# Kernel optimization log

Hardware: AMD Instinct MI355X
Metric: run time of the kernel (lower is better)

The kernel has to match this reference:

```python
import jax, jax.numpy as jnp
import numpy as np

N = 100_000      # nodes
E = 1_600_000    # edges (avg degree 16)
F_IN = 128       # num_features
HID = 64         # width
C = 40           # num_classes


def setup_inputs() -> dict:
    key = jax.random.key(0)
    ks = jax.random.split(key, 8)
    x = jax.random.normal(ks[0], (N, F_IN), jnp.float32)
    edge_index = jax.random.randint(ks[1], (2, E), 0, N, dtype=jnp.int32)
    # Xavier-uniform-like scaled weights (matches nn.init.xavier_uniform_ statistics)
    def xavier(k, fan_in, fan_out):
        lim = np.sqrt(6.0 / (fan_in + fan_out)).astype(np.float32)
        return jax.random.uniform(k, (fan_in, fan_out), jnp.float32, -lim, lim)
    return {
        "x": x,
        "edge_index": edge_index,
        "W1": xavier(ks[2], F_IN, HID), "b1": jnp.zeros((HID,), jnp.float32),
        "W2": xavier(ks[3], HID, HID),  "b2": jnp.zeros((HID,), jnp.float32),
        "W3": xavier(ks[4], HID, C),    "b3": jnp.zeros((C,), jnp.float32),
    }


def _gcn_forward(x, edge_index, W1, b1, W2, b2, W3, b3):
    n = x.shape[0]
    loops = jnp.arange(n, dtype=edge_index.dtype)
    src = jnp.concatenate([edge_index[0], loops])  # row (source)
    dst = jnp.concatenate([edge_index[1], loops])  # col (target)
    # symmetric GCN normalization with self-loops (PyG gcn_norm, edge_weight=1)
    deg = jax.ops.segment_sum(jnp.ones_like(dst, x.dtype), dst, num_segments=n)
    dis = jnp.where(deg > 0, jax.lax.rsqrt(jnp.maximum(deg, 1e-12)), 0.0)
    norm = (dis[src] * dis[dst])[:, None]  # [E+N, 1]

    def conv(h, W, b):
        h = h @ W                                                   # [n, out]
        agg = jax.ops.segment_sum(h[src] * norm, dst, num_segments=n)
        return agg + b

    h = conv(x, W1, b1)
    h = h * jax.nn.sigmoid(h)   # swish
    h = conv(h, W2, b2)
    h = h * jax.nn.sigmoid(h)   # swish
    return jax.nn.log_softmax(conv(h, W3, b3), axis=1)


def reference(x, edge_index, W1, b1, W2, b2, W3, b3):
    return _gcn_forward(x, edge_index, W1, b1, W2, b2, W3, b3)
```

## Files before the change

kernel.cpp:

```cpp
#include <hip/hip_runtime.h>
#include <math.h>

#define THREADS 256
#define S1THREADS 512
#define BSHIFT 9
#define BSIZE (1 << BSHIFT)
#define PASS1_CHUNK 2048
#define SRC_BITS 17
#define S2CAP 12288

typedef unsigned int u32;
typedef unsigned short u16;
typedef __attribute__((ext_vector_type(8))) short short8v;
typedef __attribute__((ext_vector_type(4))) float float4v;

__device__ __forceinline__ u16 f2bf(float f) {
    u32 u = __float_as_uint(f);
    u = (u + 0x7fffu + ((u >> 16) & 1u)) >> 16;
    return (u16)u;
}
__device__ __forceinline__ float bf_lo(u32 u) { return __uint_as_float(u << 16); }
__device__ __forceinline__ float bf_hi(u32 u) { return __uint_as_float(u & 0xffff0000u); }


__global__ __launch_bounds__(THREADS) void bzero_kernel(int* __restrict__ bcnt, int nbuck) {
    int i = threadIdx.x;
    if (i < nbuck) bcnt[i] = 0;
}

__global__ __launch_bounds__(THREADS) void bhist_kernel(const int* __restrict__ dst,
                                                        int* __restrict__ bcnt, int e, int nbuck) {
    __shared__ int hist[BSIZE];
    const int tid = threadIdx.x;
    const int c0  = blockIdx.x * PASS1_CHUNK;
    for (int i = tid; i < nbuck; i += THREADS) hist[i] = 0;
    __syncthreads();
    for (int i = tid; i < PASS1_CHUNK; i += THREADS) {
        int idx = c0 + i;
        if (idx < e) atomicAdd(&hist[dst[idx] >> BSHIFT], 1);
    }
    __syncthreads();
    for (int b = tid; b < nbuck; b += THREADS) {
        int h = hist[b];
        if (h) atomicAdd(&bcnt[b], h);
    }
}

__global__ __launch_bounds__(1024) void bscan_kernel(const int* __restrict__ bcnt,
                                                     int* __restrict__ bbase,
                                                     int* __restrict__ pcur,
                                                     int* __restrict__ rowptr,
                                                     int nbuck, int n, int e) {
    __shared__ int s[1024];
    int v = (threadIdx.x < nbuck) ? bcnt[threadIdx.x] : 0;
    s[threadIdx.x] = v;
    __syncthreads();
    for (int off = 1; off < 1024; off <<= 1) {
        int t = (threadIdx.x >= off) ? s[threadIdx.x - off] : 0;
        __syncthreads();
        s[threadIdx.x] += t;
        __syncthreads();
    }
    if (threadIdx.x < nbuck) {
        int ex = s[threadIdx.x] - v;
        bbase[threadIdx.x] = ex;
        pcur[threadIdx.x]  = ex;
    }
    if (threadIdx.x == 0) { bbase[nbuck] = e; rowptr[n] = e; }
}


__global__ __launch_bounds__(S1THREADS) void sort1_kernel(
    const int* __restrict__ src, const int* __restrict__ dst,
    int* __restrict__ pcur, u32* __restrict__ pairs, int e, int nbuck)
{
    __shared__ int hist[BSIZE], hist2[BSIZE], base_s[BSIZE];
    const int tid = threadIdx.x;
    const int c0  = blockIdx.x * PASS1_CHUNK;
    for (int i = tid; i < nbuck; i += S1THREADS) { hist[i] = 0; hist2[i] = 0; }
    __syncthreads();
    for (int i = tid; i < PASS1_CHUNK; i += S1THREADS) {
        int idx = c0 + i;
        if (idx < e) atomicAdd(&hist[dst[idx] >> BSHIFT], 1);
    }
    __syncthreads();
    for (int b = tid; b < nbuck; b += S1THREADS) {
        int h = hist[b];
        base_s[b] = h ? atomicAdd(&pcur[b], h) : 0;
    }
    __syncthreads();
    for (int i = tid; i < PASS1_CHUNK; i += S1THREADS) {
        int idx = c0 + i;
        if (idx < e) {
            int d = dst[idx];
            int b = d >> BSHIFT;
            int off = atomicAdd(&hist2[b], 1);
            pairs[base_s[b] + off] = ((u32)(d & (BSIZE - 1)) << SRC_BITS) | (u32)src[idx];
        }
    }
}


__global__ __launch_bounds__(S1THREADS) void sort2_kernel(
    const int* __restrict__ bbase, const u32* __restrict__ pairs,
    int* __restrict__ rowptr, float* __restrict__ dis,
    int* __restrict__ csr, int n)
{
    __shared__ int cnt[BSIZE];
    __shared__ int cur[BSIZE];
    __shared__ int s2[S1THREADS];
    __shared__ u32 pst[S2CAP];

    const int b  = blockIdx.x;
    const int d0 = b << BSHIFT;
    const int nd = min(BSIZE, n - d0);
    const int p0 = bbase[b], p1 = bbase[b + 1];
    const int sz = p1 - p0;
    const int tid = threadIdx.x;

    for (int i = tid; i < BSIZE; i += S1THREADS) cnt[i] = 0;
    __syncthreads();

    for (int j = tid; j < sz; j += S1THREADS) {
        u32 pr = pairs[p0 + j];
        if (j < S2CAP) pst[j] = pr;
        atomicAdd(&cnt[pr >> SRC_BITS], 1);
    }
    __syncthreads();

    int v = cnt[tid];
    s2[tid] = v;
    __syncthreads();
    for (int off = 1; off < S1THREADS; off <<= 1) {
        int t = (tid >= off) ? s2[tid - off] : 0;
        __syncthreads();
        s2[tid] += t;
        __syncthreads();
    }
    cur[tid] = p0 + s2[tid] - v;
    __syncthreads();

    for (int i = tid; i < nd; i += S1THREADS) {
        rowptr[d0 + i] = cur[i];
        dis[d0 + i] = rsqrtf((float)(cnt[i] + 1));
    }
    __syncthreads();

    for (int j = tid; j < sz; j += S1THREADS) {
        u32 pr = (j < S2CAP) ? pst[j] : pairs[p0 + j];
        int pos = atomicAdd(&cur[pr >> SRC_BITS], 1);
        csr[pos] = (int)(pr & ((1u << SRC_BITS) - 1));
    }
}

template <int KTOT, int OUT, int SOUT, bool PRE>
__global__ __launch_bounds__(THREADS) void mfma_gemm_kernel(
    const float* __restrict__ Xf, const u16* __restrict__ Xb,
    const float* __restrict__ W, const float* __restrict__ bin,
    const float* __restrict__ dis, u16* __restrict__ hs, int n)
{
    constexpr int NCG = (OUT + 15) / 16;
    constexpr int CC  = NCG * 16;
    constexpr int NKK = KTOT / 32;
    constexpr int WS  = KTOT + 8;

    __shared__ u16 WT[CC][WS];

    const int tid = threadIdx.x;

    for (int idx = tid; idx < KTOT * CC; idx += THREADS) {
        int k = idx / CC;
        int c = idx - k * CC;
        float v = (c < OUT) ? W[k * OUT + c] : 0.f;
        WT[c][k] = f2bf(v);
    }
    __syncthreads();

    const int lane  = tid & 63;
    const int rlane = lane & 15;
    const int kgrp  = lane >> 4;
    const int rbase = blockIdx.x * 64 + (tid >> 6) * 16;

    const int arow = min(rbase + rlane, n - 1);

    float4v acc[NCG];
#pragma unroll
    for (int g = 0; g < NCG; ++g) acc[g] = (float4v)(0.f);

    float dd_a = PRE ? dis[arow] : 0.f;

#pragma unroll
    for (int kk = 0; kk < NKK; ++kk) {
        const int kb = kk * 32 + kgrp * 8;
        short8v a;
        if (PRE) {
            uint4 u = *(const uint4*)(Xb + (size_t)arow * KTOT + kb);
            u32 w[4] = {u.x, u.y, u.z, u.w};
#pragma unroll
            for (int q = 0; q < 4; ++q) {
                float h0 = bf_lo(w[q]) * dd_a + bin[kb + 2 * q];
                float h1 = bf_hi(w[q]) * dd_a + bin[kb + 2 * q + 1];
                a[2 * q]     = (short)f2bf(h0 / (1.f + __expf(-h0)));
                a[2 * q + 1] = (short)f2bf(h1 / (1.f + __expf(-h1)));
            }
        } else {
            float4 f0 = *(const float4*)(Xf + (size_t)arow * KTOT + kb);
            float4 f1 = *(const float4*)(Xf + (size_t)arow * KTOT + kb + 4);
            a[0] = (short)f2bf(f0.x); a[1] = (short)f2bf(f0.y);
            a[2] = (short)f2bf(f0.z); a[3] = (short)f2bf(f0.w);
            a[4] = (short)f2bf(f1.x); a[5] = (short)f2bf(f1.y);
            a[6] = (short)f2bf(f1.z); a[7] = (short)f2bf(f1.w);
        }
#pragma unroll
        for (int g = 0; g < NCG; ++g) {
            short8v b = *(const short8v*)&WT[g * 16 + rlane][kb];
            acc[g] = __builtin_amdgcn_mfma_f32_16x16x32_bf16(a, b, acc[g], 0, 0, 0);
        }
    }

#pragma unroll
    for (int j = 0; j < 4; ++j) {
        int row = rbase + kgrp * 4 + j;
        if (row < n) {
            float dd = dis[row];
#pragma unroll
            for (int g = 0; g < NCG; ++g) {
                int col = g * 16 + rlane;
                if (OUT == CC || col < OUT)
                    hs[(size_t)row * SOUT + col] = f2bf(acc[g][j] * dd);
            }
        }
    }
}

__global__ __launch_bounds__(THREADS) void agg64_kernel(
    const int* __restrict__ rowptr, const int* __restrict__ csr,
    const u16* __restrict__ hs, u16* __restrict__ agg, int n)
{
    const int lane = threadIdx.x & 63;
    const int sub  = lane >> 3;
    const int gl   = lane & 7;
    const int d = (blockIdx.x * 4 + (threadIdx.x >> 6)) * 8 + sub;
    if (d >= n) return;
    const int c8 = gl * 8;

    const int beg = rowptr[d], end = rowptr[d + 1];
    float acc[8];
    {
        uint4 u = *(const uint4*)(hs + (size_t)d * 64 + c8);
        acc[0] = bf_lo(u.x); acc[1] = bf_hi(u.x);
        acc[2] = bf_lo(u.y); acc[3] = bf_hi(u.y);
        acc[4] = bf_lo(u.z); acc[5] = bf_hi(u.z);
        acc[6] = bf_lo(u.w); acc[7] = bf_hi(u.w);
    }

    int eidx = (beg + gl < end) ? csr[beg + gl] : 0;
    for (int t = beg; t < end; t += 8) {
        const int m = end - t;
        uint4 ub[8];
#pragma unroll
        for (int q = 0; q < 8; ++q) {
            int s = __shfl(eidx, (sub << 3) + q);
            if (q < m) ub[q] = *(const uint4*)(hs + (size_t)s * 64 + c8);
        }
        int eidx_n = (t + 8 + gl < end) ? csr[t + 8 + gl] : 0;
#pragma unroll
        for (int q = 0; q < 8; ++q) {
            if (q < m) {
                acc[0] += bf_lo(ub[q].x); acc[1] += bf_hi(ub[q].x);
                acc[2] += bf_lo(ub[q].y); acc[3] += bf_hi(ub[q].y);
                acc[4] += bf_lo(ub[q].z); acc[5] += bf_hi(ub[q].z);
                acc[6] += bf_lo(ub[q].w); acc[7] += bf_hi(ub[q].w);
            }
        }
        eidx = eidx_n;
    }

    uint4 o;
    o.x = (u32)f2bf(acc[0]) | ((u32)f2bf(acc[1]) << 16);
    o.y = (u32)f2bf(acc[2]) | ((u32)f2bf(acc[3]) << 16);
    o.z = (u32)f2bf(acc[4]) | ((u32)f2bf(acc[5]) << 16);
    o.w = (u32)f2bf(acc[6]) | ((u32)f2bf(acc[7]) << 16);
    *(uint4*)(agg + (size_t)d * 64 + c8) = o;
}

__global__ __launch_bounds__(THREADS) void agg40_lsm_kernel(
    const int* __restrict__ rowptr, const int* __restrict__ csr,
    const u16* __restrict__ hs, const float* __restrict__ dis,
    const float* __restrict__ b3, float* __restrict__ out, int n)
{
    constexpr int S = 48;
    const int lane = threadIdx.x & 63;
    const int sub  = lane >> 3;
    const int gl   = lane & 7;
    const int d = (blockIdx.x * 4 + (threadIdx.x >> 6)) * 8 + sub;
    if (d >= n) return;
    const bool act = (gl < 5);
    const int c8 = gl * 8;

    const int beg = rowptr[d], end = rowptr[d + 1];
    float acc[8] = {0.f,0.f,0.f,0.f,0.f,0.f,0.f,0.f};
    if (act) {
        uint4 u = *(const uint4*)(hs + (size_t)d * S + c8);
        acc[0] = bf_lo(u.x); acc[1] = bf_hi(u.x);
        acc[2] = bf_lo(u.y); acc[3] = bf_hi(u.y);
        acc[4] = bf_lo(u.z); acc[5] = bf_hi(u.z);
        acc[6] = bf_lo(u.w); acc[7] = bf_hi(u.w);
    }

    int eidx = (beg + gl < end) ? csr[beg + gl] : 0;
    for (int t = beg; t < end; t += 8) {
        const int m = end - t;
        uint4 ub[8];
#pragma unroll
        for (int q = 0; q < 8; ++q) {
            int s = __shfl(eidx, (sub << 3) + q);
            if (q < m && act) ub[q] = *(const uint4*)(hs + (size_t)s * S + c8);
        }
        int eidx_n = (t + 8 + gl < end) ? csr[t + 8 + gl] : 0;
#pragma unroll
        for (int q = 0; q < 8; ++q) {
            if (q < m && act) {
                acc[0] += bf_lo(ub[q].x); acc[1] += bf_hi(ub[q].x);
                acc[2] += bf_lo(ub[q].y); acc[3] += bf_hi(ub[q].y);
                acc[4] += bf_lo(ub[q].z); acc[5] += bf_hi(ub[q].z);
                acc[6] += bf_lo(ub[q].w); acc[7] += bf_hi(ub[q].w);
            }
        }
        eidx = eidx_n;
    }

    float val[8];
    float mx = -1e30f;
    if (act) {
        float dd = dis[d];
#pragma unroll
        for (int q = 0; q < 8; ++q) {
            val[q] = acc[q] * dd + b3[c8 + q];
            mx = fmaxf(mx, val[q]);
        }
    }
#pragma unroll
    for (int off = 4; off > 0; off >>= 1) mx = fmaxf(mx, __shfl_xor(mx, off));
    float es = 0.f;
    if (act) {
#pragma unroll
        for (int q = 0; q < 8; ++q) es += __expf(val[q] - mx);
    }
#pragma unroll
    for (int off = 4; off > 0; off >>= 1) es += __shfl_xor(es, off);
    float lse = mx + __logf(es);
    if (act) {
        float4 o0 = make_float4(val[0]-lse, val[1]-lse, val[2]-lse, val[3]-lse);
        float4 o1 = make_float4(val[4]-lse, val[5]-lse, val[6]-lse, val[7]-lse);
        *(float4*)(out + (size_t)d * 40 + c8)     = o0;
        *(float4*)(out + (size_t)d * 40 + c8 + 4) = o1;
    }
}

static inline size_t align_up(size_t v, size_t a) { return (v + a - 1) & ~(a - 1); }

extern "C" void kernel_launch(void* const* d_in, const int* in_sizes, int n_in,
                              void* d_out, int out_size, void* d_ws, size_t ws_size,
                              hipStream_t stream) {
    const float* x  = (const float*)d_in[0];
    const int*   ei = (const int*)d_in[1];
    const float* W1 = (const float*)d_in[2];
    const float* b1 = (const float*)d_in[3];
    const float* W2 = (const float*)d_in[4];
    const float* b2 = (const float*)d_in[5];
    const float* W3 = (const float*)d_in[6];
    const float* b3 = (const float*)d_in[7];
    float* out = (float*)d_out;

    const int n = in_sizes[0] / 128;
    const int e = in_sizes[1] / 2;
    const int* src = ei;
    const int* dst = ei + e;

    char* base = (char*)d_ws;
    size_t off = 0;
    float* dis = (float*)(base + off);    off = align_up(off + (size_t)n * 4, 256);
    int* rowptr = (int*)(base + off);     off = align_up(off + (size_t)(n + 1) * 4, 256);
    int* bcnt = (int*)(base + off);       off = align_up(off + 1024 * 4, 256);
    int* bbase = (int*)(base + off);      off = align_up(off + 1025 * 4, 256);
    int* pcur = (int*)(base + off);       off = align_up(off + 1024 * 4, 256);
    int* csr = (int*)(base + off);        off = align_up(off + (size_t)e * 4, 256);
    u16* hsb = (u16*)(base + off);        off = align_up(off + (size_t)n * 64 * 2, 256);
    u16* aggb = (u16*)(base + off);       off = align_up(off + (size_t)n * 64 * 2, 256);
    u32* pairs = (u32*)hsb;

    const int gb_rows = (n + 63) / 64;
    const int nbuck   = (n + BSIZE - 1) >> BSHIFT;
    const int gb_s1   = (e + PASS1_CHUNK - 1) / PASS1_CHUNK;
    const int gb_agg  = (n + 31) / 32;

    bzero_kernel<<<1, THREADS, 0, stream>>>(bcnt, nbuck);
    bhist_kernel<<<gb_s1, THREADS, 0, stream>>>(dst, bcnt, e, nbuck);
    bscan_kernel<<<1, 1024, 0, stream>>>(bcnt, bbase, pcur, rowptr, nbuck, n, e);
    sort1_kernel<<<gb_s1, S1THREADS, 0, stream>>>(src, dst, pcur, pairs, e, nbuck);
    sort2_kernel<<<nbuck, S1THREADS, 0, stream>>>(bbase, pairs, rowptr, dis, csr, n);

    mfma_gemm_kernel<128, 64, 64, false><<<gb_rows, THREADS, 0, stream>>>(
        x, nullptr, W1, nullptr, dis, hsb, n);
    agg64_kernel<<<gb_agg, THREADS, 0, stream>>>(rowptr, csr, hsb, aggb, n);

    mfma_gemm_kernel<64, 64, 64, true><<<gb_rows, THREADS, 0, stream>>>(
        nullptr, aggb, W2, b1, dis, hsb, n);
    agg64_kernel<<<gb_agg, THREADS, 0, stream>>>(rowptr, csr, hsb, aggb, n);

    mfma_gemm_kernel<64, 40, 48, true><<<gb_rows, THREADS, 0, stream>>>(
        nullptr, aggb, W3, b2, dis, hsb, n);
    agg40_lsm_kernel<<<gb_agg, THREADS, 0, stream>>>(rowptr, csr, hsb, dis, b3, out, n);
}
```

Measured before the change: 209.4 us.

## Replace atomic bucket sort with per-block histogram matrix and column scan

The CSR build now writes each block's bucket histogram into a matrix and scans it per bucket, instead of using global atomics for the counts and offsets. The zero kernel and the repeated histogram pass inside the scatter kernel go away, and the scatter order becomes deterministic. PASS1_CHUNK doubles so there are fewer blocks and a smaller matrix. In exchange it adds a colscan kernel with strided global reads and extra workspace.

```diff
diff --git a/kernel.cpp b/kernel.cpp
--- a/kernel.cpp
+++ b/kernel.cpp
@@ -5,7 +5,7 @@
 #define S1THREADS 512
 #define BSHIFT 9
 #define BSIZE (1 << BSHIFT)
-#define PASS1_CHUNK 2048
+#define PASS1_CHUNK 4096
 #define SRC_BITS 17
 #define S2CAP 12288
 
@@ -23,32 +23,52 @@
 __device__ __forceinline__ float bf_hi(u32 u) { return __uint_as_float(u & 0xffff0000u); }
 
 
-__global__ __launch_bounds__(THREADS) void bzero_kernel(int* __restrict__ bcnt, int nbuck) {
-    int i = threadIdx.x;
-    if (i < nbuck) bcnt[i] = 0;
-}
-
-__global__ __launch_bounds__(THREADS) void bhist_kernel(const int* __restrict__ dst,
-                                                        int* __restrict__ bcnt, int e, int nbuck) {
+__global__ __launch_bounds__(S1THREADS) void hist_kernel(
+    const int* __restrict__ dst, int* __restrict__ hmat, int e, int nbuck)
+{
     __shared__ int hist[BSIZE];
     const int tid = threadIdx.x;
     const int c0  = blockIdx.x * PASS1_CHUNK;
-    for (int i = tid; i < nbuck; i += THREADS) hist[i] = 0;
-    __syncthreads();
-    for (int i = tid; i < PASS1_CHUNK; i += THREADS) {
+    for (int i = tid; i < nbuck; i += S1THREADS) hist[i] = 0;
+    __syncthreads();
+    for (int i = tid; i < PASS1_CHUNK; i += S1THREADS) {
         int idx = c0 + i;
         if (idx < e) atomicAdd(&hist[dst[idx] >> BSHIFT], 1);
     }
     __syncthreads();
-    for (int b = tid; b < nbuck; b += THREADS) {
-        int h = hist[b];
-        if (h) atomicAdd(&bcnt[b], h);
-    }
-}
+    for (int b = tid; b < nbuck; b += S1THREADS)
+        hmat[blockIdx.x * nbuck + b] = hist[b];
+}
+
+
+__global__ __launch_bounds__(THREADS) void colscan_kernel(
+    const int* __restrict__ hmat, int* __restrict__ bmat,
+    int* __restrict__ bcnt, int nblk, int nbuck)
+{
+    __shared__ int s[THREADS];
+    const int b = blockIdx.x, tid = threadIdx.x;
+    int run = 0;
+    for (int t0 = 0; t0 < nblk; t0 += THREADS) {
+        int idx = t0 + tid;
+        int v = (idx < nblk) ? hmat[idx * nbuck + b] : 0;
+        s[tid] = v;
+        __syncthreads();
+        for (int off = 1; off < THREADS; off <<= 1) {
+            int t = (tid >= off) ? s[tid - off] : 0;
+            __syncthreads();
+            s[tid] += t;
+            __syncthreads();
+        }
+        if (idx < nblk) bmat[idx * nbuck + b] = run + s[tid] - v;
+        run += s[THREADS - 1];
+        __syncthreads();
+    }
+    if (tid == 0) bcnt[b] = run;
+}
+
 
 __global__ __launch_bounds__(1024) void bscan_kernel(const int* __restrict__ bcnt,
                                                      int* __restrict__ bbase,
-                                                     int* __restrict__ pcur,
                                                      int* __restrict__ rowptr,
                                                      int nbuck, int n, int e) {
     __shared__ int s[1024];
@@ -61,32 +81,22 @@
         s[threadIdx.x] += t;
         __syncthreads();
     }
-    if (threadIdx.x < nbuck) {
-        int ex = s[threadIdx.x] - v;
-        bbase[threadIdx.x] = ex;
-        pcur[threadIdx.x]  = ex;
-    }
-    if (threadIdx.x == 0) { bbase[nbuck] = e; rowptr[n] = e; }
-}
-
-
-__global__ __launch_bounds__(S1THREADS) void sort1_kernel(
+    if (threadIdx.x < nbuck) bbase[threadIdx.x] = s[threadIdx.x] - v;
+    if (threadIdx.x == 0) rowptr[n] = e;
+}
+
+
+__global__ __launch_bounds__(S1THREADS) void scatter_kernel(
     const int* __restrict__ src, const int* __restrict__ dst,
-    int* __restrict__ pcur, u32* __restrict__ pairs, int e, int nbuck)
-{
-    __shared__ int hist[BSIZE], hist2[BSIZE], base_s[BSIZE];
+    const int* __restrict__ bmat, const int* __restrict__ bbase,
+    u32* __restrict__ pairs, int e, int nbuck)
+{
+    __shared__ int base_s[BSIZE], cur[BSIZE];
     const int tid = threadIdx.x;
     const int c0  = blockIdx.x * PASS1_CHUNK;
-    for (int i = tid; i < nbuck; i += S1THREADS) { hist[i] = 0; hist2[i] = 0; }
-    __syncthreads();
-    for (int i = tid; i < PASS1_CHUNK; i += S1THREADS) {
-        int idx = c0 + i;
-        if (idx < e) atomicAdd(&hist[dst[idx] >> BSHIFT], 1);
-    }
-    __syncthreads();
     for (int b = tid; b < nbuck; b += S1THREADS) {
-        int h = hist[b];
-        base_s[b] = h ? atomicAdd(&pcur[b], h) : 0;
+        base_s[b] = bbase[b] + bmat[blockIdx.x * nbuck + b];
+        cur[b] = 0;
     }
     __syncthreads();
     for (int i = tid; i < PASS1_CHUNK; i += S1THREADS) {
@@ -94,7 +104,7 @@
         if (idx < e) {
             int d = dst[idx];
             int b = d >> BSHIFT;
-            int off = atomicAdd(&hist2[b], 1);
+            int off = atomicAdd(&cur[b], 1);
             pairs[base_s[b] + off] = ((u32)(d & (BSIZE - 1)) << SRC_BITS) | (u32)src[idx];
         }
     }
@@ -104,7 +114,7 @@
 __global__ __launch_bounds__(S1THREADS) void sort2_kernel(
     const int* __restrict__ bbase, const u32* __restrict__ pairs,
     int* __restrict__ rowptr, float* __restrict__ dis,
-    int* __restrict__ csr, int n)
+    int* __restrict__ csr, int n, int e)
 {
     __shared__ int cnt[BSIZE];
     __shared__ int cur[BSIZE];
@@ -114,7 +124,8 @@
     const int b  = blockIdx.x;
     const int d0 = b << BSHIFT;
     const int nd = min(BSIZE, n - d0);
-    const int p0 = bbase[b], p1 = bbase[b + 1];
+    const int p0 = bbase[b];
+    const int p1 = (d0 + nd >= n) ? e : bbase[b + 1];
     const int sz = p1 - p0;
     const int tid = threadIdx.x;
 
@@ -378,28 +389,30 @@
     const int* src = ei;
     const int* dst = ei + e;
 
+    const int nbuck = (n + BSIZE - 1) >> BSHIFT;
+    const int nblk  = (e + PASS1_CHUNK - 1) / PASS1_CHUNK;
+
     char* base = (char*)d_ws;
     size_t off = 0;
     float* dis = (float*)(base + off);    off = align_up(off + (size_t)n * 4, 256);
     int* rowptr = (int*)(base + off);     off = align_up(off + (size_t)(n + 1) * 4, 256);
     int* bcnt = (int*)(base + off);       off = align_up(off + 1024 * 4, 256);
     int* bbase = (int*)(base + off);      off = align_up(off + 1025 * 4, 256);
-    int* pcur = (int*)(base + off);       off = align_up(off + 1024 * 4, 256);
+    int* hmat = (int*)(base + off);       off = align_up(off + (size_t)nblk * nbuck * 4, 256);
+    int* bmat = (int*)(base + off);       off = align_up(off + (size_t)nblk * nbuck * 4, 256);
     int* csr = (int*)(base + off);        off = align_up(off + (size_t)e * 4, 256);
     u16* hsb = (u16*)(base + off);        off = align_up(off + (size_t)n * 64 * 2, 256);
     u16* aggb = (u16*)(base + off);       off = align_up(off + (size_t)n * 64 * 2, 256);
     u32* pairs = (u32*)hsb;
 
     const int gb_rows = (n + 63) / 64;
-    const int nbuck   = (n + BSIZE - 1) >> BSHIFT;
-    const int gb_s1   = (e + PASS1_CHUNK - 1) / PASS1_CHUNK;
     const int gb_agg  = (n + 31) / 32;
 
-    bzero_kernel<<<1, THREADS, 0, stream>>>(bcnt, nbuck);
-    bhist_kernel<<<gb_s1, THREADS, 0, stream>>>(dst, bcnt, e, nbuck);
-    bscan_kernel<<<1, 1024, 0, stream>>>(bcnt, bbase, pcur, rowptr, nbuck, n, e);
-    sort1_kernel<<<gb_s1, S1THREADS, 0, stream>>>(src, dst, pcur, pairs, e, nbuck);
-    sort2_kernel<<<nbuck, S1THREADS, 0, stream>>>(bbase, pairs, rowptr, dis, csr, n);
+    hist_kernel<<<nblk, S1THREADS, 0, stream>>>(dst, hmat, e, nbuck);
+    colscan_kernel<<<nbuck, THREADS, 0, stream>>>(hmat, bmat, bcnt, nblk, nbuck);
+    bscan_kernel<<<1, 1024, 0, stream>>>(bcnt, bbase, rowptr, nbuck, n, e);
+    scatter_kernel<<<nblk, S1THREADS, 0, stream>>>(src, dst, bmat, bbase, pairs, e, nbuck);
+    sort2_kernel<<<nbuck, S1THREADS, 0, stream>>>(bbase, pairs, rowptr, dis, csr, n, e);
 
     mfma_gemm_kernel<128, 64, 64, false><<<gb_rows, THREADS, 0, stream>>>(
         x, nullptr, W1, nullptr, dis, hsb, n);
```

Result: faster. 181.5 us (-13.3%).
